# Performance work log

Hardware: AMD Instinct MI355X
Metric: run time of the kernel (lower is better)

The kernel has to match this reference:

```python
import jax, jax.numpy as jnp
import numpy as np

B, N, D, H = 2, 2048, 1024, 16
HD = D // H

def setup_inputs() -> dict:
    key = jax.random.key(0)
    ks = jax.random.split(key, 8)
    s = lambda fan_in: 1.0 / np.sqrt(fan_in)
    return {
        "x": jax.random.normal(ks[0], (B, N, D), jnp.float32),
        "coverage": jax.random.uniform(ks[1], (B, N, 1), jnp.float32),
        "w_qkv": jax.random.normal(ks[2], (D, 3 * D), jnp.float32) * s(D),
        "w_out": jax.random.normal(ks[3], (D, D), jnp.float32) * s(D),
        "b_out": jnp.zeros((D,), jnp.float32),
        "w_ce1": jax.random.normal(ks[4], (1, D // 4), jnp.float32),
        "b_ce1": jnp.zeros((D // 4,), jnp.float32),
        "w_ce2": jax.random.normal(ks[5], (D // 4, H), jnp.float32) * s(D // 4),
        "b_ce2": jnp.zeros((H,), jnp.float32),
        "w_fg1": jax.random.normal(ks[6], (D, D // 4), jnp.float32) * s(D),
        "b_fg1": jnp.zeros((D // 4,), jnp.float32),
        "w_fg2": jax.random.normal(ks[7], (D // 4, 1), jnp.float32) * s(D // 4),
        "b_fg2": jnp.zeros((1,), jnp.float32),
    }

def reference(x, coverage, w_qkv, w_out, b_out, w_ce1, b_ce1, w_ce2, b_ce2,
              w_fg1, b_fg1, w_fg2, b_fg2):
    b, n, d = x.shape
    h = w_ce2.shape[1]
    hd = d // h
    scale = hd ** -0.5
    qkv = x @ w_qkv  # (B,N,3D)
    q, k, v = jnp.split(qkv, 3, axis=-1)
    q = q.reshape(b, n, h, hd).transpose(0, 2, 1, 3)  # (B,H,N,hd)
    k = k.reshape(b, n, h, hd).transpose(0, 2, 1, 3)
    v = v.reshape(b, n, h, hd).transpose(0, 2, 1, 3)
    attn = jnp.einsum("bhnd,bhmd->bhnm", q, k) * scale  # (B,H,N,N)
    # coverage bias: MLP(1 -> D/4 -> H), broadcast over query dim
    cov = jax.nn.silu(coverage @ w_ce1 + b_ce1) @ w_ce2 + b_ce2  # (B,N,H)
    cov_bias = cov.transpose(0, 2, 1)[:, :, None, :]  # (B,H,1,N)
    # fusion gate on mean-pooled features
    x_pooled = x.mean(axis=1)  # (B,D)
    g = jax.nn.sigmoid(jax.nn.silu(x_pooled @ w_fg1 + b_fg1) @ w_fg2 + b_fg2)  # (B,1)
    g = g[:, :, None, None]  # (B,1,1,1)
    # g*(attn+bias) + (1-g)*attn == attn + g*bias (exact same math)
    attn = attn + g * cov_bias
    attn = jax.nn.softmax(attn, axis=-1)
    out = jnp.einsum("bhnm,bhmd->bhnd", attn, v)  # (B,H,N,hd)
    out = out.transpose(0, 2, 1, 3).reshape(b, n, d)
    return out @ w_out + b_out
```

## Files before the change

### kernel.cpp

```cpp
#include <hip/hip_runtime.h>
#include <math.h>

typedef __bf16 bf16_t;
typedef __bf16 bf16x8 __attribute__((ext_vector_type(8)));
typedef __bf16 bf16x4 __attribute__((ext_vector_type(4)));
typedef float f32x4 __attribute__((ext_vector_type(4)));

#define MFMA16(a, b, c) __builtin_amdgcn_mfma_f32_16x16x32_bf16((a), (b), (c), 0, 0, 0)

constexpr int Bc = 2, Nc = 2048, Dc = 1024, Hc = 16, HDc = 64;
constexpr float C1 = 0.18033688011112042f;
constexpr float LOG2E = 1.4426950408889634f;

__device__ __forceinline__ void glds16(const bf16_t* g, bf16_t* l) {
    __builtin_amdgcn_global_load_lds(
        (const __attribute__((address_space(1))) unsigned int*)g,
        (__attribute__((address_space(3))) unsigned int*)l, 16, 0, 0);
}

__device__ __forceinline__ void tr64_body(const float* __restrict__ src,
                                          bf16_t* __restrict__ dst, int R, int C,
                                          int bx, int by, bf16_t* tile, int t) {
    int r0 = by * 64, c0 = bx * 64;
    int cl = t & 63, rl = t >> 6;
#pragma unroll
    for (int p = 0; p < 16; ++p) {
        int r = p * 4 + rl;
        tile[r * 66 + cl] = (bf16_t)src[(size_t)(r0 + r) * C + c0 + cl];
    }
    __syncthreads();
#pragma unroll
    for (int p = 0; p < 16; ++p) {
        int r = p * 4 + rl;
        dst[(size_t)(c0 + r) * R + r0 + cl] = tile[cl * 66 + r];
    }
}

__global__ __launch_bounds__(256) void prep(const float* __restrict__ x,
                                            bf16_t* __restrict__ Xb,
                                            const float* __restrict__ w_qkv,
                                            bf16_t* __restrict__ Wt,
                                            const float* __restrict__ w_out,
                                            bf16_t* __restrict__ WoT,
                                            float* __restrict__ pooled,
                                            const float* __restrict__ coverage,
                                            const float* __restrict__ w_ce1,
                                            const float* __restrict__ b_ce1,
                                            const float* __restrict__ w_ce2,
                                            const float* __restrict__ b_ce2,
                                            float* __restrict__ cbias) {
    __shared__ __align__(16) float smem[8768];
    int bid = blockIdx.x, t = threadIdx.x;

    if (bid < 64) {
        float* w1s = smem;
        float* b1s = smem + 256;
        float* w2s = smem + 512;
        float* part = smem + 4608;
        int b = bid >> 5, n0 = (bid & 31) * 64;
        w1s[t] = w_ce1[t];
        b1s[t] = b_ce1[t];
        {
            float4* w2v = (float4*)w2s;
            const float4* g4 = (const float4*)w_ce2;
#pragma unroll
            for (int i = 0; i < 4; ++i) w2v[i * 256 + t] = g4[i * 256 + t];
        }
        __syncthreads();
        int wv = t >> 6, lane2 = t & 63;
        float c = coverage[b * 2048 + n0 + lane2];
        float acc[16];
#pragma unroll
        for (int hh = 0; hh < 16; ++hh) acc[hh] = 0.f;
        for (int jj = 0; jj < 64; ++jj) {
            int j = wv * 64 + jj;
            float tv = fmaf(c, w1s[j], b1s[j]);
            tv = tv / (1.0f + __expf(-tv));
#pragma unroll
            for (int hh = 0; hh < 16; ++hh)
                acc[hh] = fmaf(tv, w2s[j * 16 + hh], acc[hh]);
        }
#pragma unroll
        for (int hh = 0; hh < 16; ++hh) part[lane2 * 65 + wv * 16 + hh] = acc[hh];
        __syncthreads();
#pragma unroll
        for (int i = 0; i < 4; ++i) {
            int idx = t + i * 256;
            int nl = idx >> 4, hh = idx & 15;
            const float* pr = part + nl * 65 + hh;
            float s = pr[0] + pr[16] + pr[32] + pr[48];
            cbias[((size_t)b * 16 + hh) * 2048 + n0 + nl] = LOG2E * (s + b_ce2[hh]);
        }
    } else if (bid < 832) {
        int bb = bid - 64;
        tr64_body(w_qkv, Wt, 1024, 3072, bb % 48, bb / 48, (bf16_t*)smem, t);
    } else if (bid < 1088) {
        int bb = bid - 832;
        tr64_body(w_out, WoT, 1024, 1024, bb & 15, bb >> 4, (bf16_t*)smem, t);
    } else {
        int blk = bid - 1088;
        int b = blk >> 7;
        int rbase = blk * 16;
        int d = t * 4;
        float s0 = 0.f, s1 = 0.f, s2 = 0.f, s3 = 0.f;
        for (int rr = 0; rr < 16; ++rr) {
            size_t off = (size_t)(rbase + rr) * 1024 + d;
            float4 v = *(const float4*)(x + off);
            s0 += v.x; s1 += v.y; s2 += v.z; s3 += v.w;
            bf16x4 o = { (bf16_t)v.x, (bf16_t)v.y, (bf16_t)v.z, (bf16_t)v.w };
            *(bf16x4*)(Xb + off) = o;
        }
        atomicAdd(&pooled[b * 1024 + d + 0], s0);
        atomicAdd(&pooled[b * 1024 + d + 1], s1);
        atomicAdd(&pooled[b * 1024 + d + 2], s2);
        atomicAdd(&pooled[b * 1024 + d + 3], s3);
    }
}

__global__ __launch_bounds__(256) void qkv_gemm(const bf16_t* __restrict__ Xb,
                                                const bf16_t* __restrict__ Wt,
                                                bf16_t* __restrict__ Q,
                                                bf16_t* __restrict__ Kb,
                                                bf16_t* __restrict__ Vt,
                                                const float* __restrict__ pooled,
                                                const float* __restrict__ w_fg1,
                                                const float* __restrict__ b_fg1,
                                                const float* __restrict__ w_fg2,
                                                float* __restrict__ hacc) {
    __shared__ __align__(16) bf16_t At[3][128 * 32];
    __shared__ __align__(16) bf16_t Bt[3][128 * 32];
    int t = threadIdx.x;

    if (blockIdx.y == 24) {
        __shared__ float red[4];
        int blk = blockIdx.x;
        int b = blk >> 4, jb = (blk & 15) * 16;
        for (int jj = 0; jj < 16; ++jj) {
            int j = jb + jj;
            float p = 0.f;
#pragma unroll
            for (int i = 0; i < 4; ++i) {
                int d = t * 4 + i;
                p += pooled[b * 1024 + d] * w_fg1[d * 256 + j];
            }
#pragma unroll
            for (int off = 32; off > 0; off >>= 1) p += __shfl_down(p, off);
            if ((t & 63) == 0) red[t >> 6] = p;
            __syncthreads();
            if (t == 0) {
                float hj = (red[0] + red[1] + red[2] + red[3]) * (1.0f / 2048.0f) + b_fg1[j];
                hj = hj / (1.0f + __expf(-hj));
                atomicAdd(&hacc[b], hj * w_fg2[j]);
            }
            __syncthreads();
        }
        return;
    }

    int w = t >> 6, lane = t & 63;
    int l16 = lane & 15, quad = lane >> 4;
    int wm = w & 1, wx = w >> 1;
    int m0 = blockIdx.x * 128;
    int n0 = blockIdx.y * 128;
    f32x4 acc[4][4] = {};
    int sw = (l16 >> 2) & 3;

    int arow[2], asc[2], aoff[2];
#pragma unroll
    for (int i = 0; i < 2; ++i) {
        int fb = i * 4096 + w * 1024;
        int f = fb + lane * 16;
        int row = f >> 6;
        int ch = (f >> 4) & 3;
        arow[i] = row;
        asc[i] = ch ^ ((row >> 2) & 3);
        aoff[i] = fb >> 1;
    }
    auto stage = [&](int k0, int bf) {
#pragma unroll
        for (int i = 0; i < 2; ++i) {
            glds16(Wt + (size_t)(n0 + arow[i]) * 1024 + k0 + asc[i] * 8, At[bf] + aoff[i]);
            glds16(Xb + (size_t)(m0 + arow[i]) * 1024 + k0 + asc[i] * 8, Bt[bf] + aoff[i]);
        }
    };

    stage(0, 0);
    stage(32, 1);
    int cur = 0, nxt = 2;
    for (int ks = 0; ks < 32; ++ks) {
        if (ks + 1 < 32) {
            asm volatile("s_waitcnt vmcnt(4)" ::: "memory");
        } else {
            asm volatile("s_waitcnt vmcnt(0)" ::: "memory");
        }
        __builtin_amdgcn_s_barrier();
        if (ks + 2 < 32) stage((ks + 2) * 32, nxt);
        __builtin_amdgcn_sched_barrier(0);

        const bf16_t* Ab = At[cur];
        const bf16_t* Bb = Bt[cur];
        bf16x8 afr[4], bfr[4];
#pragma unroll
        for (int mi = 0; mi < 4; ++mi)
            afr[mi] = *(const bf16x8*)(Ab + (wm * 64 + mi * 16 + l16) * 32 + ((quad ^ sw) * 8));
#pragma unroll
        for (int ni = 0; ni < 4; ++ni)
            bfr[ni] = *(const bf16x8*)(Bb + (wx * 64 + ni * 16 + l16) * 32 + ((quad ^ sw) * 8));
        __builtin_amdgcn_s_setprio(1);
#pragma unroll
        for (int mi = 0; mi < 4; ++mi)
#pragma unroll
            for (int ni = 0; ni < 4; ++ni)
                acc[mi][ni] = MFMA16(afr[mi], bfr[ni], acc[mi][ni]);
        __builtin_amdgcn_s_setprio(0);
        cur = (cur == 2) ? 0 : cur + 1;
        nxt = (nxt == 2) ? 0 : nxt + 1;
    }

    int sec = n0 >> 10;
    float scq = (sec == 0) ? C1 : 1.0f;
#pragma unroll
    for (int mi = 0; mi < 4; ++mi) {
        int gc = n0 + wm * 64 + mi * 16 + quad * 4;
        int dcol = gc & 1023;
        int h = dcol >> 6, hd = dcol & 63;
#pragma unroll
        for (int ni = 0; ni < 4; ++ni) {
            int gx = m0 + wx * 64 + ni * 16 + l16;
            int b = gx >> 11, n = gx & 2047;
            size_t bh = (size_t)(b * 16 + h);
            if (sec == 2) {
#pragma unroll
                for (int r = 0; r < 4; ++r)
                    Vt[(bh * 64 + hd + r) * 2048 + n] = (bf16_t)acc[mi][ni][r];
            } else {
                bf16x4 pk = { (bf16_t)(acc[mi][ni][0] * scq), (bf16_t)(acc[mi][ni][1] * scq),
                              (bf16_t)(acc[mi][ni][2] * scq), (bf16_t)(acc[mi][ni][3] * scq) };
                bf16_t* dst = (sec == 0 ? Q : Kb);
                *(bf16x4*)(dst + (bh * 2048 + n) * 64 + hd) = pk;
            }
        }
    }
}

__global__ __launch_bounds__(256) void attn_k(const bf16_t* __restrict__ Q,
                                              const bf16_t* __restrict__ Kb,
                                              const bf16_t* __restrict__ Vt,
                                              const float* __restrict__ cbias,
                                              const float* __restrict__ hacc,
                                              const float* __restrict__ b_fg2,
                                              bf16_t* __restrict__ O) {
    __shared__ __align__(16) bf16_t kbuf[3][64 * 64];
    __shared__ __align__(16) bf16_t vbuf[3][64 * 64];
    __shared__ __align__(16) float ball[2048];
    int t = threadIdx.x, w = t >> 6, lane = t & 63;
    int l16 = lane & 15, quad = lane >> 4;
    int bh = blockIdx.y;
    int b = bh >> 4, h = bh & 15;
    int qa = blockIdx.x * 128 + w * 32;
    const bf16_t* Qh = Q + (size_t)bh * 2048 * 64;
    const bf16_t* Kh = Kb + (size_t)bh * 2048 * 64;
    const bf16_t* Vh = Vt + (size_t)bh * 64 * 2048;
    const float* bih = cbias + (size_t)bh * 2048;
    float g = 1.0f / (1.0f + __expf(-(hacc[b] + b_fg2[0])));

#pragma unroll
    for (int c = 0; c < 2; ++c) {
        float4 v = *(const float4*)(bih + c * 1024 + t * 4);
        float4 sv = { v.x * g, v.y * g, v.z * g, v.w * g };
        *(float4*)(ball + c * 1024 + t * 4) = sv;
    }

    int fb0 = w * 2048, fb1 = fb0 + 1024;
    int f0 = fb0 + lane * 16, f1 = fb1 + lane * 16;
    int krow0 = f0 >> 7, kch0 = ((f0 >> 4) & 7) ^ (krow0 & 7);
    int krow1 = f1 >> 7, kch1 = ((f1 >> 4) & 7) ^ (krow1 & 7);

    bf16x8 qf[2][2];
#pragma unroll
    for (int qt = 0; qt < 2; ++qt)
#pragma unroll
        for (int dh = 0; dh < 2; ++dh)
            qf[qt][dh] = *(const bf16x8*)(Qh + (size_t)(qa + qt * 16 + l16) * 64 + dh * 32 + quad * 8);

    f32x4 o[2][4] = {};
    f32x4 lacc[2] = {};
    bf16x8 onesb;
#pragma unroll
    for (int i = 0; i < 8; ++i) onesb[i] = (bf16_t)1.0f;
    int swl = l16 & 7;
    int qh = quad >> 1, ql = quad & 1;

    int bk0 = l16 * 64 + ((quad ^ swl) * 8);
    int bk1 = l16 * 64 + (((4 + quad) ^ swl) * 8);
    int bv0 = l16 * 64 + ql * 4 + ((qh ^ swl) * 8);
    int bv1 = l16 * 64 + ql * 4 + (((2 + qh) ^ swl) * 8);
    int bv2 = l16 * 64 + ql * 4 + (((4 + qh) ^ swl) * 8);
    int bv3 = l16 * 64 + ql * 4 + (((6 + qh) ^ swl) * 8);

    auto stage = [&](int tile_, int bf) {
        int jn = tile_ * 64;
        glds16(Kh + (size_t)(jn + krow0) * 64 + kch0 * 8, &kbuf[bf][fb0 >> 1]);
        glds16(Kh + (size_t)(jn + krow1) * 64 + kch1 * 8, &kbuf[bf][fb1 >> 1]);
        glds16(Vh + (size_t)krow0 * 2048 + jn + kch0 * 8, &vbuf[bf][fb0 >> 1]);
        glds16(Vh + (size_t)krow1 * 2048 + jn + kch1 * 8, &vbuf[bf][fb1 >> 1]);
    };

    stage(0, 0);
    stage(1, 1);
    asm volatile("s_waitcnt lgkmcnt(0)" ::: "memory");
    int cur = 0, nxt = 2;

    for (int it = 0; it < 32; ++it) {
        int j0 = it * 64;
        if (it + 1 < 32) {
            asm volatile("s_waitcnt vmcnt(4)" ::: "memory");
        } else {
            asm volatile("s_waitcnt vmcnt(0)" ::: "memory");
        }
        __builtin_amdgcn_s_barrier();
        if (it + 2 < 32) stage(it + 2, nxt);
        __builtin_amdgcn_sched_barrier(0);

        const bf16_t* kb = &kbuf[cur][0];
        const bf16_t* vb = &vbuf[cur][0];

        f32x4 s[2][4];
        __builtin_amdgcn_s_setprio(1);
#pragma unroll
        for (int kt = 0; kt < 4; ++kt) {
            f32x4 bi = *(const f32x4*)(ball + j0 + kt * 16 + quad * 4);
            bf16x8 kf0 = *(const bf16x8*)(kb + kt * 1024 + bk0);
            bf16x8 kf1 = *(const bf16x8*)(kb + kt * 1024 + bk1);
#pragma unroll
            for (int qt = 0; qt < 2; ++qt) {
                s[qt][kt] = MFMA16(kf0, qf[qt][0], bi);
                s[qt][kt] = MFMA16(kf1, qf[qt][1], s[qt][kt]);
            }
        }
        __builtin_amdgcn_s_setprio(0);

        bf16x8 pf[2][2];
#pragma unroll
        for (int qt = 0; qt < 2; ++qt) {
#pragma unroll
            for (int kt = 0; kt < 4; ++kt)
#pragma unroll
                for (int r = 0; r < 4; ++r)
                    s[qt][kt][r] = __builtin_amdgcn_exp2f(s[qt][kt][r]);
#pragma unroll
            for (int pv = 0; pv < 2; ++pv) {
                bf16x8 tmp;
#pragma unroll
                for (int i = 0; i < 4; ++i) {
                    tmp[i]     = (bf16_t)s[qt][2 * pv][i];
                    tmp[i + 4] = (bf16_t)s[qt][2 * pv + 1][i];
                }
                pf[qt][pv] = tmp;
            }
        }

        __builtin_amdgcn_s_setprio(1);
#pragma unroll
        for (int qt = 0; qt < 2; ++qt) {
            lacc[qt] = MFMA16(pf[qt][0], onesb, lacc[qt]);
            lacc[qt] = MFMA16(pf[qt][1], onesb, lacc[qt]);
        }
#pragma unroll
        for (int dt = 0; dt < 4; ++dt) {
            bf16x4 va0 = *(const bf16x4*)(vb + dt * 1024 + bv0);
            bf16x4 vc0 = *(const bf16x4*)(vb + dt * 1024 + bv1);
            bf16x8 vf0 = __builtin_shufflevector(va0, vc0, 0, 1, 2, 3, 4, 5, 6, 7);
            bf16x4 va1 = *(const bf16x4*)(vb + dt * 1024 + bv2);
            bf16x4 vc1 = *(const bf16x4*)(vb + dt * 1024 + bv3);
            bf16x8 vf1 = __builtin_shufflevector(va1, vc1, 0, 1, 2, 3, 4, 5, 6, 7);
#pragma unroll
            for (int qt = 0; qt < 2; ++qt) {
                o[qt][dt] = MFMA16(pf[qt][0], vf0, o[qt][dt]);
                o[qt][dt] = MFMA16(pf[qt][1], vf1, o[qt][dt]);
            }
        }
        __builtin_amdgcn_s_setprio(0);
        cur = (cur == 2) ? 0 : cur + 1;
        nxt = (nxt == 2) ? 0 : nxt + 1;
    }

#pragma unroll
    for (int qt = 0; qt < 2; ++qt) {
        f32x4 rinv;
#pragma unroll
        for (int r = 0; r < 4; ++r) rinv[r] = 1.0f / lacc[qt][r];
#pragma unroll
        for (int dt = 0; dt < 4; ++dt)
#pragma unroll
            for (int r = 0; r < 4; ++r) {
                int row = qa + qt * 16 + quad * 4 + r;
                O[(size_t)(b * 2048 + row) * 1024 + h * 64 + dt * 16 + l16] =
                    (bf16_t)(o[qt][dt][r] * rinv[r]);
            }
    }
}

__global__ __launch_bounds__(256) void out_gemm(const bf16_t* __restrict__ A,
                                                const bf16_t* __restrict__ Wt,
                                                const float* __restrict__ bias,
                                                float* __restrict__ Cout) {
    __shared__ __align__(16) bf16_t At[3][128 * 32];
    __shared__ __align__(16) bf16_t Bt[3][128 * 32];
    int t = threadIdx.x, w = t >> 6, lane = t & 63;
    int l16 = lane & 15, quad = lane >> 4;
    int wm = w & 1, wx = w >> 1;
    int m0 = blockIdx.x * 128;
    int n0 = blockIdx.y * 128;
    f32x4 acc[4][4] = {};
    int sw = (l16 >> 2) & 3;

    int arow[2], asc[2], aoff[2];
#pragma unroll
    for (int i = 0; i < 2; ++i) {
        int fb = i * 4096 + w * 1024;
        int f = fb + lane * 16;
        int row = f >> 6;
        int ch = (f >> 4) & 3;
        arow[i] = row;
        asc[i] = ch ^ ((row >> 2) & 3);
        aoff[i] = fb >> 1;
    }
    auto stage = [&](int k0, int bf) {
#pragma unroll
        for (int i = 0; i < 2; ++i) {
            glds16(Wt + (size_t)(n0 + arow[i]) * 1024 + k0 + asc[i] * 8, At[bf] + aoff[i]);
            glds16(A + (size_t)(m0 + arow[i]) * 1024 + k0 + asc[i] * 8, Bt[bf] + aoff[i]);
        }
    };

    stage(0, 0);
    stage(32, 1);
    int cur = 0, nxt = 2;
    for (int ks = 0; ks < 32; ++ks) {
        if (ks + 1 < 32) {
            asm volatile("s_waitcnt vmcnt(4)" ::: "memory");
        } else {
            asm volatile("s_waitcnt vmcnt(0)" ::: "memory");
        }
        __builtin_amdgcn_s_barrier();
        if (ks + 2 < 32) stage((ks + 2) * 32, nxt);
        __builtin_amdgcn_sched_barrier(0);

        const bf16_t* Ab = At[cur];
        const bf16_t* Bb = Bt[cur];
        bf16x8 afr[4], bfr[4];
#pragma unroll
        for (int mi = 0; mi < 4; ++mi)
            afr[mi] = *(const bf16x8*)(Ab + (wm * 64 + mi * 16 + l16) * 32 + ((quad ^ sw) * 8));
#pragma unroll
        for (int ni = 0; ni < 4; ++ni)
            bfr[ni] = *(const bf16x8*)(Bb + (wx * 64 + ni * 16 + l16) * 32 + ((quad ^ sw) * 8));
        __builtin_amdgcn_s_setprio(1);
#pragma unroll
        for (int mi = 0; mi < 4; ++mi)
#pragma unroll
            for (int ni = 0; ni < 4; ++ni)
                acc[mi][ni] = MFMA16(afr[mi], bfr[ni], acc[mi][ni]);
        __builtin_amdgcn_s_setprio(0);
        cur = (cur == 2) ? 0 : cur + 1;
        nxt = (nxt == 2) ? 0 : nxt + 1;
    }

#pragma unroll
    for (int mi = 0; mi < 4; ++mi) {
        int gc = n0 + wm * 64 + mi * 16 + quad * 4;
        float4 bv = *(const float4*)(bias + gc);
#pragma unroll
        for (int ni = 0; ni < 4; ++ni) {
            int gx = m0 + wx * 64 + ni * 16 + l16;
            float4 ov = { acc[mi][ni][0] + bv.x, acc[mi][ni][1] + bv.y,
                          acc[mi][ni][2] + bv.z, acc[mi][ni][3] + bv.w };
            *(float4*)(Cout + (size_t)gx * 1024 + gc) = ov;
        }
    }
}

extern "C" void kernel_launch(void* const* d_in, const int* in_sizes, int n_in,
                              void* d_out, int out_size, void* d_ws, size_t ws_size,
                              hipStream_t stream) {
    const float* x     = (const float*)d_in[0];
    const float* cov   = (const float*)d_in[1];
    const float* w_qkv = (const float*)d_in[2];
    const float* w_out = (const float*)d_in[3];
    const float* b_out = (const float*)d_in[4];
    const float* w_ce1 = (const float*)d_in[5];
    const float* b_ce1 = (const float*)d_in[6];
    const float* w_ce2 = (const float*)d_in[7];
    const float* b_ce2 = (const float*)d_in[8];
    const float* w_fg1 = (const float*)d_in[9];
    const float* b_fg1 = (const float*)d_in[10];
    const float* w_fg2 = (const float*)d_in[11];
    const float* b_fg2 = (const float*)d_in[12];

    char* ws = (char*)d_ws;
    bf16_t* Wt     = (bf16_t*)(ws);
    bf16_t* WoT    = (bf16_t*)(ws + 6291456);
    bf16_t* Xb     = (bf16_t*)(ws + 8388608);
    bf16_t* Qb     = (bf16_t*)(ws + 16777216);
    bf16_t* Kbb    = (bf16_t*)(ws + 25165824);
    bf16_t* Vt     = (bf16_t*)(ws + 33554432);
    bf16_t* Ob     = (bf16_t*)(ws + 41943040);
    float*  pooled = (float*)(ws + 50331648);
    float*  hacc   = (float*)(ws + 50339840);
    float*  biasb  = (float*)(ws + 50340096);

    hipMemsetAsync(pooled, 0, 8200, stream);
    prep<<<1344, 256, 0, stream>>>(x, Xb, w_qkv, Wt, w_out, WoT, pooled,
                                   cov, w_ce1, b_ce1, w_ce2, b_ce2, biasb);
    qkv_gemm<<<dim3(32, 25), 256, 0, stream>>>(Xb, Wt, Qb, Kbb, Vt,
                                               pooled, w_fg1, b_fg1, w_fg2, hacc);
    attn_k<<<dim3(16, 32), 256, 0, stream>>>(Qb, Kbb, Vt, biasb, hacc, b_fg2, Ob);
    out_gemm<<<dim3(32, 8), 256, 0, stream>>>(Ob, WoT, b_out, (float*)d_out);
}
```

Baseline: 246.3 us.

## Reduce LDS buffering depth and remap attention blocks by XCD

Drops the triple-buffered LDS pipelines in the QKV GEMM and attention kernel to double buffering, issuing the next tile's loads after a barrier each iteration. The output GEMM loses its software pipeline entirely and becomes a synchronous load-then-compute loop. The attention grid is flattened to 1D and remapped so each XCD handles four contiguous batch-heads, which should improve L2 reuse of K/V. Less LDS may allow higher occupancy, but there is less latency hiding, more barriers per iteration, and the output GEMM no longer overlaps its global loads with compute.

```diff
diff --git a/kernel.cpp b/kernel.cpp
--- a/kernel.cpp
+++ b/kernel.cpp
@@ -127,8 +127,8 @@
                                                 const float* __restrict__ b_fg1,
                                                 const float* __restrict__ w_fg2,
                                                 float* __restrict__ hacc) {
-    __shared__ __align__(16) bf16_t At[3][128 * 32];
-    __shared__ __align__(16) bf16_t Bt[3][128 * 32];
+    __shared__ __align__(16) bf16_t At[2][128 * 32];
+    __shared__ __align__(16) bf16_t Bt[2][128 * 32];
     int t = threadIdx.x;
 
     if (blockIdx.y == 24) {
@@ -185,20 +185,21 @@
     };
 
     stage(0, 0);
-    stage(32, 1);
-    int cur = 0, nxt = 2;
     for (int ks = 0; ks < 32; ++ks) {
+        int sel = ks & 1;
+        asm volatile("s_waitcnt lgkmcnt(0)" ::: "memory");
+        __builtin_amdgcn_s_barrier();
         if (ks + 1 < 32) {
+            stage((ks + 1) * 32, sel ^ 1);
             asm volatile("s_waitcnt vmcnt(4)" ::: "memory");
         } else {
             asm volatile("s_waitcnt vmcnt(0)" ::: "memory");
         }
         __builtin_amdgcn_s_barrier();
-        if (ks + 2 < 32) stage((ks + 2) * 32, nxt);
         __builtin_amdgcn_sched_barrier(0);
 
-        const bf16_t* Ab = At[cur];
-        const bf16_t* Bb = Bt[cur];
+        const bf16_t* Ab = At[sel];
+        const bf16_t* Bb = Bt[sel];
         bf16x8 afr[4], bfr[4];
 #pragma unroll
         for (int mi = 0; mi < 4; ++mi)
@@ -213,8 +214,6 @@
             for (int ni = 0; ni < 4; ++ni)
                 acc[mi][ni] = MFMA16(afr[mi], bfr[ni], acc[mi][ni]);
         __builtin_amdgcn_s_setprio(0);
-        cur = (cur == 2) ? 0 : cur + 1;
-        nxt = (nxt == 2) ? 0 : nxt + 1;
     }
 
     int sec = n0 >> 10;
@@ -250,14 +249,17 @@
                                               const float* __restrict__ hacc,
                                               const float* __restrict__ b_fg2,
                                               bf16_t* __restrict__ O) {
-    __shared__ __align__(16) bf16_t kbuf[3][64 * 64];
-    __shared__ __align__(16) bf16_t vbuf[3][64 * 64];
+    __shared__ __align__(16) bf16_t kbuf[2][64 * 64];
+    __shared__ __align__(16) bf16_t vbuf[2][64 * 64];
     __shared__ __align__(16) float ball[2048];
     int t = threadIdx.x, w = t >> 6, lane = t & 63;
     int l16 = lane & 15, quad = lane >> 4;
-    int bh = blockIdx.y;
+    int id = blockIdx.x;
+    int xcd = id & 7, slot = id >> 3;
+    int bh = xcd * 4 + (slot >> 4);
+    int xblk = slot & 15;
     int b = bh >> 4, h = bh & 15;
-    int qa = blockIdx.x * 128 + w * 32;
+    int qa = xblk * 128 + w * 32;
     const bf16_t* Qh = Q + (size_t)bh * 2048 * 64;
     const bf16_t* Kh = Kb + (size_t)bh * 2048 * 64;
     const bf16_t* Vh = Vt + (size_t)bh * 64 * 2048;
@@ -307,23 +309,22 @@
     };
 
     stage(0, 0);
-    stage(1, 1);
-    asm volatile("s_waitcnt lgkmcnt(0)" ::: "memory");
-    int cur = 0, nxt = 2;
 
     for (int it = 0; it < 32; ++it) {
-        int j0 = it * 64;
+        int sel = it & 1, j0 = it * 64;
+        asm volatile("s_waitcnt lgkmcnt(0)" ::: "memory");
+        __builtin_amdgcn_s_barrier();
         if (it + 1 < 32) {
+            stage(it + 1, sel ^ 1);
             asm volatile("s_waitcnt vmcnt(4)" ::: "memory");
         } else {
             asm volatile("s_waitcnt vmcnt(0)" ::: "memory");
         }
         __builtin_amdgcn_s_barrier();
-        if (it + 2 < 32) stage(it + 2, nxt);
         __builtin_amdgcn_sched_barrier(0);
 
-        const bf16_t* kb = &kbuf[cur][0];
-        const bf16_t* vb = &vbuf[cur][0];
+        const bf16_t* kb = &kbuf[sel][0];
+        const bf16_t* vb = &vbuf[sel][0];
 
         f32x4 s[2][4];
         __builtin_amdgcn_s_setprio(1);
@@ -381,8 +382,6 @@
             }
         }
         __builtin_amdgcn_s_setprio(0);
-        cur = (cur == 2) ? 0 : cur + 1;
-        nxt = (nxt == 2) ? 0 : nxt + 1;
     }
 
 #pragma unroll
@@ -405,8 +404,8 @@
                                                 const bf16_t* __restrict__ Wt,
                                                 const float* __restrict__ bias,
                                                 float* __restrict__ Cout) {
-    __shared__ __align__(16) bf16_t At[3][128 * 32];
-    __shared__ __align__(16) bf16_t Bt[3][128 * 32];
+    __shared__ __align__(16) bf16_t At[128 * 32];
+    __shared__ __align__(16) bf16_t Bt[128 * 32];
     int t = threadIdx.x, w = t >> 6, lane = t & 63;
     int l16 = lane & 15, quad = lane >> 4;
     int wm = w & 1, wx = w >> 1;
@@ -415,56 +414,31 @@
     f32x4 acc[4][4] = {};
     int sw = (l16 >> 2) & 3;
 
-    int arow[2], asc[2], aoff[2];
-#pragma unroll
-    for (int i = 0; i < 2; ++i) {
-        int fb = i * 4096 + w * 1024;
-        int f = fb + lane * 16;
-        int row = f >> 6;
-        int ch = (f >> 4) & 3;
-        arow[i] = row;
-        asc[i] = ch ^ ((row >> 2) & 3);
-        aoff[i] = fb >> 1;
-    }
-    auto stage = [&](int k0, int bf) {
+    for (int k0 = 0; k0 < 1024; k0 += 32) {
 #pragma unroll
         for (int i = 0; i < 2; ++i) {
-            glds16(Wt + (size_t)(n0 + arow[i]) * 1024 + k0 + asc[i] * 8, At[bf] + aoff[i]);
-            glds16(A + (size_t)(m0 + arow[i]) * 1024 + k0 + asc[i] * 8, Bt[bf] + aoff[i]);
-        }
-    };
-
-    stage(0, 0);
-    stage(32, 1);
-    int cur = 0, nxt = 2;
-    for (int ks = 0; ks < 32; ++ks) {
-        if (ks + 1 < 32) {
-            asm volatile("s_waitcnt vmcnt(4)" ::: "memory");
-        } else {
-            asm volatile("s_waitcnt vmcnt(0)" ::: "memory");
-        }
-        __builtin_amdgcn_s_barrier();
-        if (ks + 2 < 32) stage((ks + 2) * 32, nxt);
-        __builtin_amdgcn_sched_barrier(0);
-
-        const bf16_t* Ab = At[cur];
-        const bf16_t* Bb = Bt[cur];
+            int fb = i * 4096 + w * 1024;
+            int f = fb + lane * 16;
+            int row = f >> 6;
+            int ch = (f >> 4) & 3;
+            int sc = ch ^ ((row >> 2) & 3);
+            glds16(Wt + (size_t)(n0 + row) * 1024 + k0 + sc * 8, At + (fb >> 1));
+            glds16(A + (size_t)(m0 + row) * 1024 + k0 + sc * 8, Bt + (fb >> 1));
+        }
+        __syncthreads();
         bf16x8 afr[4], bfr[4];
 #pragma unroll
         for (int mi = 0; mi < 4; ++mi)
-            afr[mi] = *(const bf16x8*)(Ab + (wm * 64 + mi * 16 + l16) * 32 + ((quad ^ sw) * 8));
+            afr[mi] = *(const bf16x8*)(At + (wm * 64 + mi * 16 + l16) * 32 + ((quad ^ sw) * 8));
 #pragma unroll
         for (int ni = 0; ni < 4; ++ni)
-            bfr[ni] = *(const bf16x8*)(Bb + (wx * 64 + ni * 16 + l16) * 32 + ((quad ^ sw) * 8));
-        __builtin_amdgcn_s_setprio(1);
+            bfr[ni] = *(const bf16x8*)(Bt + (wx * 64 + ni * 16 + l16) * 32 + ((quad ^ sw) * 8));
 #pragma unroll
         for (int mi = 0; mi < 4; ++mi)
 #pragma unroll
             for (int ni = 0; ni < 4; ++ni)
                 acc[mi][ni] = MFMA16(afr[mi], bfr[ni], acc[mi][ni]);
-        __builtin_amdgcn_s_setprio(0);
-        cur = (cur == 2) ? 0 : cur + 1;
-        nxt = (nxt == 2) ? 0 : nxt + 1;
+        __syncthreads();
     }
 
 #pragma unroll
@@ -515,6 +489,6 @@
                                    cov, w_ce1, b_ce1, w_ce2, b_ce2, biasb);
     qkv_gemm<<<dim3(32, 25), 256, 0, stream>>>(Xb, Wt, Qb, Kbb, Vt,
                                                pooled, w_fg1, b_fg1, w_fg2, hacc);
-    attn_k<<<dim3(16, 32), 256, 0, stream>>>(Qb, Kbb, Vt, biasb, hacc, b_fg2, Ob);
+    attn_k<<<512, 256, 0, stream>>>(Qb, Kbb, Vt, biasb, hacc, b_fg2, Ob);
     out_gemm<<<dim3(32, 8), 256, 0, stream>>>(Ob, WoT, b_out, (float*)d_out);
 }
```

Result: faster. 240.5 us (-2.4%).
